# Kernel tuning notes

Hardware: AMD Instinct MI355X
Metric: run time of the kernel (lower is better)

The kernel has to match this reference:

```python
import jax, jax.numpy as jnp
import numpy as np

N_NODES = 50000
N_EDGES = 800000
D_IN = 128
D_OUT = 128


def setup_inputs() -> dict:
    key = jax.random.key(0)
    ks = jax.random.split(key, 10)
    x = jax.random.normal(ks[0], (N_NODES, D_IN), dtype=jnp.float32)
    lp_rows = jax.random.randint(ks[1], (N_EDGES,), 0, N_NODES, dtype=jnp.int32)
    lp_cols = jax.random.randint(ks[2], (N_EDGES,), 0, N_NODES, dtype=jnp.int32)
    # low-pass operator: positive normalized-adjacency-like weights
    lp_vals = jax.random.uniform(ks[3], (N_EDGES,), dtype=jnp.float32) / 16.0
    hp_rows = jax.random.randint(ks[4], (N_EDGES,), 0, N_NODES, dtype=jnp.int32)
    hp_cols = jax.random.randint(ks[5], (N_EDGES,), 0, N_NODES, dtype=jnp.int32)
    # high-pass operator: signed (Laplacian-like) weights
    hp_vals = jax.random.normal(ks[6], (N_EDGES,), dtype=jnp.float32) / 16.0
    alpha_w = jax.random.normal(ks[7], (1, D_IN), dtype=jnp.float32) * 0.05
    alpha_b = jnp.zeros((1,), dtype=jnp.float32)
    W = jax.random.normal(ks[8], (D_OUT, D_IN), dtype=jnp.float32) * (1.0 / np.sqrt(D_IN))
    b = jnp.zeros((D_OUT,), dtype=jnp.float32)
    return {"x": x, "lp_rows": lp_rows, "lp_cols": lp_cols, "lp_vals": lp_vals,
            "hp_rows": hp_rows, "hp_cols": hp_cols, "hp_vals": hp_vals,
            "alpha_w": alpha_w, "alpha_b": alpha_b, "W": W, "b": b}


def _spmm(rows, cols, vals, x, n):
    # COO sparse-dense matmul: out[r] += vals[e] * x[cols[e]]
    return jax.ops.segment_sum(vals[:, None] * x[cols], rows, num_segments=n)


def reference(x, lp_rows, lp_cols, lp_vals, hp_rows, hp_cols, hp_vals,
              alpha_w, alpha_b, W, b):
    n = x.shape[0]
    # per-node mixing gate: alpha_i = sigmoid(x_i . theta + b)  -> [N, 1]
    alpha = jax.nn.sigmoid(x @ alpha_w.T + alpha_b)
    z_lp = _spmm(lp_rows, lp_cols, lp_vals, x, n)   # [N, D_IN]
    z_hp = _spmm(hp_rows, hp_cols, hp_vals, x, n)   # [N, D_IN]
    z_mix = alpha * z_lp + (1.0 - alpha) * z_hp
    out = jax.nn.relu(z_mix @ W.T + b)              # use_activation=True
    return out, alpha
```

## Files before the change

### kernel.cpp

```cpp
#include <hip/hip_runtime.h>

#define N_NODES_C 50000
#define N_EDGES_C 800000
#define N_EDGES2_C (2 * N_EDGES_C)
#define D 128
#define NSHARD 8
#define SCAP 16
#define OFCAP 4096

static __device__ __forceinline__ unsigned short f2bf(float f) {
  unsigned u = __float_as_uint(f);
  u += 0x7fff + ((u >> 16) & 1);
  return (unsigned short)(u >> 16);
}
static __device__ __forceinline__ float bf_lo(unsigned u) {
  return __uint_as_float(u << 16);
}
static __device__ __forceinline__ float bf_hi(unsigned u) {
  return __uint_as_float(u & 0xffff0000u);
}

static __device__ __forceinline__ int xcd_id() {
  int v;
  asm volatile("s_getreg_b32 %0, hwreg(HW_REG_XCC_ID, 0, 4)" : "=s"(v));
  return v & (NSHARD - 1);
}

__global__ __launch_bounds__(256) void fill_kernel(
    const int* __restrict__ lp_rows, const int* __restrict__ lp_cols,
    const float* __restrict__ lp_vals,
    const int* __restrict__ hp_rows, const int* __restrict__ hp_cols,
    const float* __restrict__ hp_vals,
    const float* __restrict__ alpha,
    int* __restrict__ rcursor,
    unsigned* __restrict__ pairs,
    int* __restrict__ ofcnt,
    uint2* __restrict__ ofl) {
  int e = blockIdx.x * 256 + threadIdx.x;
  if (e >= N_EDGES2_C) return;
  int xcc = xcd_id();
  int r, c;
  float v;
  if (e < N_EDGES_C) {
    r = lp_rows[e];
    c = lp_cols[e];
    v = lp_vals[e] * alpha[r];
  } else {
    int i = e - N_EDGES_C;
    r = hp_rows[i];
    c = hp_cols[i];
    v = hp_vals[i] * (1.0f - alpha[r]);
  }
  int p = atomicAdd(&rcursor[xcc * N_NODES_C + r], 1);
  if (p < SCAP) {
    unsigned pk = (unsigned)c | ((unsigned)f2bf(v) << 16);
    pairs[((size_t)r << 7) + (xcc << 4) + p] = pk;
  } else {
    int q = atomicAdd(ofcnt, 1);
    if (q < OFCAP)
      ofl[q] = make_uint2(((unsigned)r << 16) | (unsigned)c,
                          (unsigned)__float_as_int(v));
  }
}

#define GNODES 64
#define GP 16
#define LDP 132

__global__ __launch_bounds__(256) void gemm_y_kernel(
    const float* __restrict__ x,
    const float* __restrict__ W,
    const float* __restrict__ aw,
    const float* __restrict__ ab,
    unsigned* __restrict__ y,
    float* __restrict__ alpha_out,
    float* __restrict__ alpha_ws,
    int n) {
  __shared__ float wt[D][LDP];
  __shared__ float zs[GP][LDP];

  int t = threadIdx.x;
  int lane = t & 63;
  int node0 = blockIdx.x * GNODES;

  float awv0 = aw[lane];
  float awv1 = aw[lane + 64];
  float ab0 = ab[0];

  #pragma unroll
  for (int it = 0; it < 16; ++it) {
    int f = t + it * 256;
    int j = f >> 5;
    int k4 = f & 31;
    *(float4*)&wt[j][k4 * 4] = ((const float4*)W)[f];
  }

  int tj = t >> 3;
  int ns = t & 7;
  int j0 = tj * 2;

  for (int p = 0; p < 4; ++p) {
    int nb = node0 + p * GP;
    __syncthreads();
    #pragma unroll
    for (int it = 0; it < 2; ++it) {
      int f = t + it * 256;
      int r = f >> 5;
      int c4 = f & 31;
      int node = nb + r;
      float4 v = make_float4(0.f, 0.f, 0.f, 0.f);
      if (node < n) v = ((const float4*)(x + (size_t)node * D))[c4];
      *(float4*)&zs[r][c4 * 4] = v;
    }
    __syncthreads();

    if (t < 64) {
      for (int r = 0; r < GP; ++r) {
        float s = zs[r][lane] * awv0 + zs[r][lane + 64] * awv1;
        #pragma unroll
        for (int off = 32; off > 0; off >>= 1)
          s += __shfl_down(s, off);
        int node = nb + r;
        if (lane == 0 && node < n) {
          float a = 1.0f / (1.0f + __expf(-(s + ab0)));
          alpha_out[node] = a;
          alpha_ws[node] = a;
        }
      }
    }

    float acc[2][4] = {};
    #pragma unroll 4
    for (int k = 0; k < D; k += 4) {
      float4 w0 = *(const float4*)&wt[j0][k];
      float4 w1 = *(const float4*)&wt[j0 + 1][k];
      float4 w2 = *(const float4*)&wt[j0 + 64][k];
      float4 w3 = *(const float4*)&wt[j0 + 65][k];
      float4 z0 = *(const float4*)&zs[ns * 2 + 0][k];
      float4 z1 = *(const float4*)&zs[ns * 2 + 1][k];
      acc[0][0] += z0.x * w0.x + z0.y * w0.y + z0.z * w0.z + z0.w * w0.w;
      acc[0][1] += z0.x * w1.x + z0.y * w1.y + z0.z * w1.z + z0.w * w1.w;
      acc[0][2] += z0.x * w2.x + z0.y * w2.y + z0.z * w2.z + z0.w * w2.w;
      acc[0][3] += z0.x * w3.x + z0.y * w3.y + z0.z * w3.z + z0.w * w3.w;
      acc[1][0] += z1.x * w0.x + z1.y * w0.y + z1.z * w0.z + z1.w * w0.w;
      acc[1][1] += z1.x * w1.x + z1.y * w1.y + z1.z * w1.z + z1.w * w1.w;
      acc[1][2] += z1.x * w2.x + z1.y * w2.y + z1.z * w2.z + z1.w * w2.w;
      acc[1][3] += z1.x * w3.x + z1.y * w3.y + z1.z * w3.z + z1.w * w3.w;
    }

    #pragma unroll
    for (int ii = 0; ii < 2; ++ii) {
      int node = nb + ns * 2 + ii;
      if (node < n) {
        uint2 o;
        o.x = (unsigned)f2bf(acc[ii][0]) | ((unsigned)f2bf(acc[ii][2]) << 16);
        o.y = (unsigned)f2bf(acc[ii][1]) | ((unsigned)f2bf(acc[ii][3]) << 16);
        *(uint2*)&y[(size_t)node * 64 + j0] = o;
      }
    }
  }
}

__global__ __launch_bounds__(256) void gather_kernel(
    const int* __restrict__ rcursor,
    const unsigned* __restrict__ pairs,
    const unsigned* __restrict__ y,
    const float* __restrict__ bias,
    const int* __restrict__ ofcnt,
    const uint2* __restrict__ ofl,
    float* __restrict__ out) {
  int row = (int)((blockIdx.x * blockDim.x + threadIdx.x) >> 6);
  int lane = threadIdx.x & 63;
  if (row >= N_NODES_C) return;

  const unsigned* rp = pairs + ((size_t)row << 7);
  unsigned w0 = rp[lane];
  unsigned w1 = rp[64 + lane];

  float aL = 0.f, aH = 0.f;
  #pragma unroll
  for (int s = 0; s < NSHARD; ++s) {
    int ds = rcursor[(size_t)s * N_NODES_C + row];
    if (ds > SCAP) ds = SCAP;
    unsigned wsrc = (s < 4) ? w0 : w1;
    int base = (s & 3) << 4;
    int p = 0;
    for (; p + 1 < ds; p += 2) {
      unsigned pk0 = (unsigned)__shfl((int)wsrc, base + p);
      unsigned pk1 = (unsigned)__shfl((int)wsrc, base + p + 1);
      unsigned u0 = y[(size_t)(pk0 & 0xffffu) * 64 + lane];
      unsigned u1 = y[(size_t)(pk1 & 0xffffu) * 64 + lane];
      float v0 = bf_hi(pk0);
      float v1 = bf_hi(pk1);
      aL += v0 * bf_lo(u0) + v1 * bf_lo(u1);
      aH += v0 * bf_hi(u0) + v1 * bf_hi(u1);
    }
    if (p < ds) {
      unsigned pk = (unsigned)__shfl((int)wsrc, base + p);
      unsigned u = y[(size_t)(pk & 0xffffu) * 64 + lane];
      aL += bf_hi(pk) * bf_lo(u);
      aH += bf_hi(pk) * bf_hi(u);
    }
  }

  int nof = *ofcnt;
  if (nof > OFCAP) nof = OFCAP;
  for (int i = 0; i < nof; ++i) {
    uint2 o = ofl[i];
    if ((int)(o.x >> 16) == row) {
      unsigned u = y[(size_t)(o.x & 0xffffu) * 64 + lane];
      float v = __int_as_float((int)o.y);
      aL += v * bf_lo(u);
      aH += v * bf_hi(u);
    }
  }

  out[(size_t)row * D + lane] = fmaxf(aL + bias[lane], 0.0f);
  out[(size_t)row * D + lane + 64] = fmaxf(aH + bias[lane + 64], 0.0f);
}

extern "C" void kernel_launch(void* const* d_in, const int* in_sizes, int n_in,
                              void* d_out, int out_size, void* d_ws, size_t ws_size,
                              hipStream_t stream) {
  const float* x = (const float*)d_in[0];
  const int* lp_rows = (const int*)d_in[1];
  const int* lp_cols = (const int*)d_in[2];
  const float* lp_vals = (const float*)d_in[3];
  const int* hp_rows = (const int*)d_in[4];
  const int* hp_cols = (const int*)d_in[5];
  const float* hp_vals = (const float*)d_in[6];
  const float* alpha_w = (const float*)d_in[7];
  const float* alpha_b = (const float*)d_in[8];
  const float* W = (const float*)d_in[9];
  const float* bias = (const float*)d_in[10];

  float* out = (float*)d_out;
  float* alpha_out = out + (size_t)N_NODES_C * D;

  char* ws = (char*)d_ws;
  unsigned* y = (unsigned*)ws;   ws += (size_t)N_NODES_C * 64 * 4;
  float* alpha_ws = (float*)ws;  ws += 200192;
  int* rcursor = (int*)ws;       ws += (size_t)N_NODES_C * NSHARD * 4;
  int* ofcnt = (int*)ws;         ws += 256;
  uint2* ofl = (uint2*)ws;       ws += (size_t)OFCAP * 8;
  unsigned* pairs = (unsigned*)ws;
  ws += (size_t)N_NODES_C * NSHARD * SCAP * 4;

  hipMemsetAsync(rcursor, 0,
                 (size_t)N_NODES_C * NSHARD * sizeof(int) + 256, stream);

  gemm_y_kernel<<<(N_NODES_C + GNODES - 1) / GNODES, 256, 0, stream>>>(
      x, W, alpha_w, alpha_b, y, alpha_out, alpha_ws, N_NODES_C);

  fill_kernel<<<(N_EDGES2_C + 255) / 256, 256, 0, stream>>>(
      lp_rows, lp_cols, lp_vals, hp_rows, hp_cols, hp_vals,
      alpha_ws, rcursor, pairs, ofcnt, ofl);

  gather_kernel<<<(N_NODES_C * 64 + 255) / 256, 256, 0, stream>>>(
      rcursor, pairs, (const unsigned*)y, bias, ofcnt, ofl, out);
}
```

Measured before the change: 331.9 us.

## Split alpha into own kernel and fuse edge bucketing into GEMM kernel

Moves the sigmoid gate computation into a small standalone kernel (one wave per node) and merges the edge-bucketing fill pass into the tail of the projection GEMM kernel. Each GEMM block now also processes a contiguous chunk of edges after finishing its node tile. The aim is to overlap the atomic-heavy scatter with the compute-bound GEMM and drop the serial alpha loop from the GEMM blocks. In exchange it adds a kernel launch, re-reads x for alpha, and the edge loop is limited to 256 threads per block with large per-block chunks, which may reduce latency hiding.

```diff
diff --git a/kernel.cpp b/kernel.cpp
--- a/kernel.cpp
+++ b/kernel.cpp
@@ -8,6 +8,12 @@
 #define SCAP 16
 #define OFCAP 4096
 
+#define GNODES 64
+#define GP 16
+#define LDP 132
+#define GRID ((N_NODES_C + GNODES - 1) / GNODES)
+#define EPB ((N_EDGES2_C + GRID - 1) / GRID)
+
 static __device__ __forceinline__ unsigned short f2bf(float f) {
   unsigned u = __float_as_uint(f);
   u += 0x7fff + ((u >> 16) & 1);
@@ -26,7 +32,32 @@
   return v & (NSHARD - 1);
 }
 
-__global__ __launch_bounds__(256) void fill_kernel(
+__global__ __launch_bounds__(256) void alpha_kernel(
+    const float* __restrict__ x,
+    const float* __restrict__ aw,
+    const float* __restrict__ ab,
+    float* __restrict__ alpha_out,
+    float* __restrict__ alpha_ws,
+    int n) {
+  int wave = (int)((blockIdx.x * blockDim.x + threadIdx.x) >> 6);
+  int lane = threadIdx.x & 63;
+  if (wave >= n) return;
+  const float* xr = x + (size_t)wave * D;
+  float s = xr[lane] * aw[lane] + xr[lane + 64] * aw[lane + 64];
+  #pragma unroll
+  for (int off = 32; off > 0; off >>= 1)
+    s += __shfl_down(s, off);
+  if (lane == 0) {
+    float a = 1.0f / (1.0f + __expf(-(s + ab[0])));
+    alpha_out[wave] = a;
+    alpha_ws[wave] = a;
+  }
+}
+
+__global__ __launch_bounds__(256) void gemm_fill_kernel(
+    const float* __restrict__ x,
+    const float* __restrict__ W,
+    unsigned* __restrict__ y,
     const int* __restrict__ lp_rows, const int* __restrict__ lp_cols,
     const float* __restrict__ lp_vals,
     const int* __restrict__ hp_rows, const int* __restrict__ hp_cols,
@@ -35,57 +66,13 @@
     int* __restrict__ rcursor,
     unsigned* __restrict__ pairs,
     int* __restrict__ ofcnt,
-    uint2* __restrict__ ofl) {
-  int e = blockIdx.x * 256 + threadIdx.x;
-  if (e >= N_EDGES2_C) return;
-  int xcc = xcd_id();
-  int r, c;
-  float v;
-  if (e < N_EDGES_C) {
-    r = lp_rows[e];
-    c = lp_cols[e];
-    v = lp_vals[e] * alpha[r];
-  } else {
-    int i = e - N_EDGES_C;
-    r = hp_rows[i];
-    c = hp_cols[i];
-    v = hp_vals[i] * (1.0f - alpha[r]);
-  }
-  int p = atomicAdd(&rcursor[xcc * N_NODES_C + r], 1);
-  if (p < SCAP) {
-    unsigned pk = (unsigned)c | ((unsigned)f2bf(v) << 16);
-    pairs[((size_t)r << 7) + (xcc << 4) + p] = pk;
-  } else {
-    int q = atomicAdd(ofcnt, 1);
-    if (q < OFCAP)
-      ofl[q] = make_uint2(((unsigned)r << 16) | (unsigned)c,
-                          (unsigned)__float_as_int(v));
-  }
-}
-
-#define GNODES 64
-#define GP 16
-#define LDP 132
-
-__global__ __launch_bounds__(256) void gemm_y_kernel(
-    const float* __restrict__ x,
-    const float* __restrict__ W,
-    const float* __restrict__ aw,
-    const float* __restrict__ ab,
-    unsigned* __restrict__ y,
-    float* __restrict__ alpha_out,
-    float* __restrict__ alpha_ws,
+    uint2* __restrict__ ofl,
     int n) {
   __shared__ float wt[D][LDP];
   __shared__ float zs[GP][LDP];
 
   int t = threadIdx.x;
-  int lane = t & 63;
   int node0 = blockIdx.x * GNODES;
-
-  float awv0 = aw[lane];
-  float awv1 = aw[lane + 64];
-  float ab0 = ab[0];
 
   #pragma unroll
   for (int it = 0; it < 16; ++it) {
@@ -113,21 +100,6 @@
       *(float4*)&zs[r][c4 * 4] = v;
     }
     __syncthreads();
-
-    if (t < 64) {
-      for (int r = 0; r < GP; ++r) {
-        float s = zs[r][lane] * awv0 + zs[r][lane + 64] * awv1;
-        #pragma unroll
-        for (int off = 32; off > 0; off >>= 1)
-          s += __shfl_down(s, off);
-        int node = nb + r;
-        if (lane == 0 && node < n) {
-          float a = 1.0f / (1.0f + __expf(-(s + ab0)));
-          alpha_out[node] = a;
-          alpha_ws[node] = a;
-        }
-      }
-    }
 
     float acc[2][4] = {};
     #pragma unroll 4
@@ -159,6 +131,35 @@
       }
     }
   }
+
+  int xcc = xcd_id();
+  int e0 = blockIdx.x * EPB;
+  int e1 = e0 + EPB;
+  if (e1 > N_EDGES2_C) e1 = N_EDGES2_C;
+  for (int e = e0 + t; e < e1; e += 256) {
+    int r, c;
+    float v;
+    if (e < N_EDGES_C) {
+      r = lp_rows[e];
+      c = lp_cols[e];
+      v = lp_vals[e] * alpha[r];
+    } else {
+      int i = e - N_EDGES_C;
+      r = hp_rows[i];
+      c = hp_cols[i];
+      v = hp_vals[i] * (1.0f - alpha[r]);
+    }
+    int p = atomicAdd(&rcursor[xcc * N_NODES_C + r], 1);
+    if (p < SCAP) {
+      unsigned pk = (unsigned)c | ((unsigned)f2bf(v) << 16);
+      pairs[((size_t)r << 7) + (xcc << 4) + p] = pk;
+    } else {
+      int q = atomicAdd(ofcnt, 1);
+      if (q < OFCAP)
+        ofl[q] = make_uint2(((unsigned)r << 16) | (unsigned)c,
+                            (unsigned)__float_as_int(v));
+    }
+  }
 }
 
 __global__ __launch_bounds__(256) void gather_kernel(
@@ -249,12 +250,13 @@
   hipMemsetAsync(rcursor, 0,
                  (size_t)N_NODES_C * NSHARD * sizeof(int) + 256, stream);
 
-  gemm_y_kernel<<<(N_NODES_C + GNODES - 1) / GNODES, 256, 0, stream>>>(
-      x, W, alpha_w, alpha_b, y, alpha_out, alpha_ws, N_NODES_C);
-
-  fill_kernel<<<(N_EDGES2_C + 255) / 256, 256, 0, stream>>>(
+  alpha_kernel<<<(N_NODES_C + 3) / 4, 256, 0, stream>>>(
+      x, alpha_w, alpha_b, alpha_out, alpha_ws, N_NODES_C);
+
+  gemm_fill_kernel<<<GRID, 256, 0, stream>>>(
+      x, W, y,
       lp_rows, lp_cols, lp_vals, hp_rows, hp_cols, hp_vals,
-      alpha_ws, rcursor, pairs, ofcnt, ofl);
+      alpha_ws, rcursor, pairs, ofcnt, ofl, N_NODES_C);
 
   gather_kernel<<<(N_NODES_C * 64 + 255) / 256, 256, 0, stream>>>(
       rcursor, pairs, (const unsigned*)y, bias, ofcnt, ofl, out);
```

After: 306.3 us. -7.7%, faster.
